# Kernel optimization log

Measured on AMD Instinct MI355X. Metric: run time of the kernel, lower is better.

## Reference

```python
import jax, jax.numpy as jnp
import numpy as np

N = 100000      # nodes
E = 1600000     # edges
F = 64          # num_features
C = 10          # num_classes
L = 4           # num_layers
B = 128         # graphs in batch


def setup_inputs() -> dict:
    key = jax.random.key(0)
    ks = jax.random.split(key, 8)
    x = jax.random.normal(ks[0], (N, F), dtype=jnp.float32)
    edge_index = jax.random.randint(ks[1], (2, E), 0, N, dtype=jnp.int64)
    batch = jnp.sort(jax.random.randint(ks[2], (N,), 0, B, dtype=jnp.int64))
    scale = 1.0 / jnp.sqrt(jnp.float32(F))
    W1s = jax.random.normal(ks[3], (L, F, F), dtype=jnp.float32) * scale
    W2s = jax.random.normal(ks[4], (L, F, F), dtype=jnp.float32) * scale
    fc_w = jax.random.normal(ks[5], (C, F), dtype=jnp.float32) * scale
    fc_b = jax.random.normal(ks[6], (C,), dtype=jnp.float32) * 0.01
    return {"x": x, "edge_index": edge_index, "batch": batch,
            "W1s": W1s, "W2s": W2s, "fc_w": fc_w, "fc_b": fc_b}


def reference(x, edge_index, batch, W1s, W2s, fc_w, fc_b):
    src, dst = edge_index[0], edge_index[1]
    h = x
    for l in range(L):  # small fixed layer count
        # GINConv, eps=0: (1+eps)*x + sum of neighbor features (gather + scatter-add)
        agg = jax.ops.segment_sum(h[src], dst, num_segments=N)
        h = agg + h
        # MLP([F,F,F], bias=False, plain_last=False, act=sigmoid): two linears, each followed by sigmoid
        h = jax.nn.sigmoid(h @ W1s[l])
        h = jax.nn.sigmoid(h @ W2s[l])
    # global_add_pool over graphs in the batch
    xr = jax.ops.segment_sum(h, batch, num_segments=B)  # [B, F]
    logits = xr @ fc_w.T + fc_b                          # [B, C]
    return jax.nn.log_softmax(logits, axis=1), xr
```

## Files before the change

kernel.cpp:

```cpp
#include <hip/hip_runtime.h>
#include <hip/hip_bf16.h>

#define NN 100000
#define NE 1600000
#define FF 64
#define NC 10
#define NL 4
#define NB 128
#define LDST 72
#define CAP 48
#define NW 196
#define WCAPE 8704
#define NCHUNK ((NE + 1023) / 1024)
#define XF_BLOCKS (NN * FF / 2048)
#define CONV_BLOCKS (2 * NL * FF * FF / 256)

typedef __attribute__((ext_vector_type(8))) short short8;
typedef __attribute__((ext_vector_type(8))) unsigned short ushort8;
typedef __attribute__((ext_vector_type(4))) float f32x4;
typedef __attribute__((ext_vector_type(2))) float f32x2;

static __device__ __forceinline__ unsigned short f2bf(float x) {
  unsigned int u = __float_as_uint(x);
  unsigned int r = (u + 0x7fffu + ((u >> 16) & 1u)) >> 16;
  return (unsigned short)r;
}
static __device__ __forceinline__ float bf2f(unsigned short u) {
  return __uint_as_float(((unsigned int)u) << 16);
}
static __device__ __forceinline__ uint2 pack_f8(const float* a) {
  int w0 = __builtin_amdgcn_cvt_pk_fp8_f32(a[0], a[1], 0, false);
  w0 = __builtin_amdgcn_cvt_pk_fp8_f32(a[2], a[3], w0, true);
  int w1 = __builtin_amdgcn_cvt_pk_fp8_f32(a[4], a[5], 0, false);
  w1 = __builtin_amdgcn_cvt_pk_fp8_f32(a[6], a[7], w1, true);
  return make_uint2((unsigned)w0, (unsigned)w1);
}
static __device__ __forceinline__ void acc8(f32x2* a, uint2 v) {
#if __has_builtin(__builtin_amdgcn_cvt_pk_f32_fp8)
  a[0] += __builtin_amdgcn_cvt_pk_f32_fp8((int)v.x, false);
  a[1] += __builtin_amdgcn_cvt_pk_f32_fp8((int)v.x, true);
  a[2] += __builtin_amdgcn_cvt_pk_f32_fp8((int)v.y, false);
  a[3] += __builtin_amdgcn_cvt_pk_f32_fp8((int)v.y, true);
#else
  a[0][0] += __builtin_amdgcn_cvt_f32_fp8((int)v.x, 0);
  a[0][1] += __builtin_amdgcn_cvt_f32_fp8((int)v.x, 1);
  a[1][0] += __builtin_amdgcn_cvt_f32_fp8((int)v.x, 2);
  a[1][1] += __builtin_amdgcn_cvt_f32_fp8((int)v.x, 3);
  a[2][0] += __builtin_amdgcn_cvt_f32_fp8((int)v.y, 0);
  a[2][1] += __builtin_amdgcn_cvt_f32_fp8((int)v.y, 1);
  a[3][0] += __builtin_amdgcn_cvt_f32_fp8((int)v.y, 2);
  a[3][1] += __builtin_amdgcn_cvt_f32_fp8((int)v.y, 3);
#endif
}
static __device__ __forceinline__ unsigned char f2f8(float v) {
  return (unsigned char)(__builtin_amdgcn_cvt_pk_fp8_f32(v, v, 0, false) & 0xff);
}

__global__ __launch_bounds__(256) void prep_kernel(
    const float* __restrict__ x, const float* __restrict__ W1s,
    const float* __restrict__ W2s, uint2* __restrict__ xf8,
    unsigned short* __restrict__ Wt, int* __restrict__ wcnt,
    uint2* __restrict__ hf8a, uint2* __restrict__ hf8b,
    float* __restrict__ xr) {
  int b = blockIdx.x;
  if (b < XF_BLOCKS) {
    int t = b * 256 + threadIdx.x;
    size_t base = (size_t)t * 8;
    float4 a = *(const float4*)(x + base);
    float4 c = *(const float4*)(x + base + 4);
    float f[8] = {a.x, a.y, a.z, a.w, c.x, c.y, c.z, c.w};
    xf8[t] = pack_f8(f);
  } else if (b < XF_BLOCKS + CONV_BLOCKS) {
    int t = (b - XF_BLOCKS) * 256 + threadIdx.x;
    int mat = t >> 12, idx = t & 4095;
    int k = idx >> 6, n = idx & 63;
    int l = mat >> 1;
    const float* W = (mat & 1) ? (W2s + (size_t)l * FF * FF) : (W1s + (size_t)l * FF * FF);
    Wt[(size_t)mat * FF * FF + n * FF + k] = f2bf(W[k * FF + n]);
  } else {
    int c = threadIdx.x;
    float4 z = make_float4(0.f, 0.f, 0.f, 0.f);
    #pragma unroll
    for (int k = 0; k < 8; ++k)
      *(float4*)(xr + c * 32 + k * 4) = z;
    if (c < NW) wcnt[c] = 0;
    if (c < 8) {
      xf8[(size_t)NN * 8 + c] = make_uint2(0, 0);
      hf8a[(size_t)NN * 8 + c] = make_uint2(0, 0);
      hf8b[(size_t)NN * 8 + c] = make_uint2(0, 0);
    }
  }
}

__global__ __launch_bounds__(256) void binB_kernel(const int* __restrict__ src,
                                                   const int* __restrict__ dst,
                                                   int* __restrict__ wcnt,
                                                   unsigned int* __restrict__ ebuf) {
  __shared__ int lcnt[NW];
  __shared__ int lbase[NW];
  int t = threadIdx.x;
  int base = blockIdx.x * 1024 + t * 4;
  int d[4], s[4], wj[4];
  bool v[4];
  #pragma unroll
  for (int j = 0; j < 4; ++j) {
    int e = base + j;
    v[j] = (e < NE);
    d[j] = v[j] ? dst[e] : 0;
    s[j] = v[j] ? src[e] : 0;
    wj[j] = d[j] >> 9;
  }
  for (int i = t; i < NW; i += 256) lcnt[i] = 0;
  __syncthreads();
  #pragma unroll
  for (int j = 0; j < 4; ++j)
    if (v[j]) atomicAdd(&lcnt[wj[j]], 1);
  __syncthreads();
  if (t < NW) {
    lbase[t] = atomicAdd(&wcnt[t], lcnt[t]);
    lcnt[t] = 0;
  }
  __syncthreads();
  #pragma unroll
  for (int j = 0; j < 4; ++j) {
    if (v[j]) {
      int pos = lbase[wj[j]] + atomicAdd(&lcnt[wj[j]], 1);
      if (pos < WCAPE)
        ebuf[(size_t)wj[j] * WCAPE + pos] =
            ((unsigned)(d[j] & 511) << 17) | (unsigned)s[j];
    }
  }
}

__global__ __launch_bounds__(256) void fillC_kernel(const unsigned int* __restrict__ ebuf,
                                                    const int* __restrict__ wcnt,
                                                    int* __restrict__ csr,
                                                    int* __restrict__ deg) {
  __shared__ int cur[512];
  int b = blockIdx.x;
  int t = threadIdx.x;
  int n0 = b << 9;
  cur[t] = 0; cur[t + 256] = 0;
  __syncthreads();
  int cnt = min(wcnt[b], WCAPE);
  const unsigned int* ep = ebuf + (size_t)b * WCAPE;
  for (int i = t; i < cnt; i += 256) {
    unsigned int e = ep[i];
    int dl = e >> 17;
    int s = (int)(e & 0x1ffffu);
    int slot = atomicAdd(&cur[dl], 1);
    if (slot < CAP) csr[(n0 + dl) * CAP + slot] = s;
  }
  __syncthreads();
  #pragma unroll
  for (int p = 0; p < 2; ++p) {
    int nl = p * 256 + t;
    int node = n0 + nl;
    if (node < NN) {
      int c = min(cur[nl], CAP);
      deg[node] = c;
      int end = (c + 3) & ~3;
      for (; c < end; ++c) csr[node * CAP + c] = NN;
    }
  }
}

__global__ __launch_bounds__(256) void layer_kernel(
    const uint2* __restrict__ hin8, const int* __restrict__ csr,
    const int* __restrict__ deg, const unsigned short* __restrict__ Wt,
    uint2* __restrict__ hout8, const int* __restrict__ batch,
    float* __restrict__ xr, int last) {
  __shared__ __align__(16) unsigned short uL[64 * LDST];
  __shared__ __align__(8) unsigned char fb[64 * 64];
  int t = threadIdx.x;
  int row0 = blockIdx.x * 64;
  int lane = t & 63, w = t >> 6;
  int j = lane & 7;
  int gnode = lane >> 3;

  #pragma unroll
  for (int pass = 0; pass < 2; ++pass) {
    int r = w * 16 + pass * 8 + gnode;
    int node = row0 + r;
    f32x2 a[4] = {{0.f, 0.f}, {0.f, 0.f}, {0.f, 0.f}, {0.f, 0.f}};
    if (node < NN) {
      const uint2* hp = hin8 + j;
      acc8(a, hp[(size_t)node * 8]);
      int i = node * CAP;
      int dg = deg[node];
      int endp = i + ((dg + 3) & ~3);
      for (; i + 8 <= endp; i += 8) {
        int4 x0 = *(const int4*)(csr + i);
        int4 x1 = *(const int4*)(csr + i + 4);
        uint2 r0 = hp[(size_t)x0.x * 8];
        uint2 r1 = hp[(size_t)x0.y * 8];
        uint2 r2 = hp[(size_t)x0.z * 8];
        uint2 r3 = hp[(size_t)x0.w * 8];
        uint2 r4 = hp[(size_t)x1.x * 8];
        uint2 r5 = hp[(size_t)x1.y * 8];
        uint2 r6 = hp[(size_t)x1.z * 8];
        uint2 r7 = hp[(size_t)x1.w * 8];
        acc8(a, r0); acc8(a, r1); acc8(a, r2); acc8(a, r3);
        acc8(a, r4); acc8(a, r5); acc8(a, r6); acc8(a, r7);
      }
      if (i < endp) {
        int4 x0 = *(const int4*)(csr + i);
        uint2 r0 = hp[(size_t)x0.x * 8];
        uint2 r1 = hp[(size_t)x0.y * 8];
        uint2 r2 = hp[(size_t)x0.z * 8];
        uint2 r3 = hp[(size_t)x0.w * 8];
        acc8(a, r0); acc8(a, r1); acc8(a, r2); acc8(a, r3);
      }
    }
    ushort8 u;
    #pragma unroll
    for (int kk = 0; kk < 8; ++kk) u[kk] = f2bf(a[kk >> 1][kk & 1]);
    *(ushort8*)(&uL[r * LDST + j * 8]) = u;
  }

  __builtin_amdgcn_sched_barrier(0);

  int m = lane & 15, q = lane >> 4;
  short8 b1[4][2], b2[4][2];
  #pragma unroll
  for (int c4 = 0; c4 < 4; ++c4) {
    #pragma unroll
    for (int s = 0; s < 2; ++s) {
      b1[c4][s] = *(const short8*)(Wt + (c4 * 16 + m) * FF + s * 32 + q * 8);
      b2[c4][s] = *(const short8*)(Wt + FF * FF + (c4 * 16 + m) * FF + s * 32 + q * 8);
    }
  }

  f32x4 acc[4] = {{0,0,0,0},{0,0,0,0},{0,0,0,0},{0,0,0,0}};
  #pragma unroll
  for (int s = 0; s < 2; ++s) {
    short8 a = *(const short8*)(&uL[(w * 16 + m) * LDST + s * 32 + q * 8]);
    #pragma unroll
    for (int c4 = 0; c4 < 4; ++c4)
      acc[c4] = __builtin_amdgcn_mfma_f32_16x16x32_bf16(a, b1[c4][s], acc[c4], 0, 0, 0);
  }
  #pragma unroll
  for (int c4 = 0; c4 < 4; ++c4) {
    #pragma unroll
    for (int i = 0; i < 4; ++i) {
      int r = w * 16 + q * 4 + i;
      float sgv = 1.f / (1.f + __expf(-acc[c4][i]));
      uL[r * LDST + c4 * 16 + m] = f2bf(sgv);
    }
  }

  f32x4 acc2[4] = {{0,0,0,0},{0,0,0,0},{0,0,0,0},{0,0,0,0}};
  #pragma unroll
  for (int s = 0; s < 2; ++s) {
    short8 a = *(const short8*)(&uL[(w * 16 + m) * LDST + s * 32 + q * 8]);
    #pragma unroll
    for (int c4 = 0; c4 < 4; ++c4)
      acc2[c4] = __builtin_amdgcn_mfma_f32_16x16x32_bf16(a, b2[c4][s], acc2[c4], 0, 0, 0);
  }
  if (last) {
    #pragma unroll
    for (int c4 = 0; c4 < 4; ++c4) {
      #pragma unroll
      for (int i = 0; i < 4; ++i) {
        int r = w * 16 + q * 4 + i;
        float sgv = 1.f / (1.f + __expf(-acc2[c4][i]));
        uL[r * LDST + c4 * 16 + m] = f2bf(sgv);
      }
    }
    int r0 = w * 16;
    int node0 = row0 + r0;
    if (node0 < NN) {
      float pacc = 0.f;
      int cur = batch[node0];
      #pragma unroll
      for (int r = 0; r < 16; ++r) {
        int node = node0 + r;
        if (node < NN) {
          int bb = batch[node];
          if (bb != cur) {
            unsafeAtomicAdd(&xr[(size_t)cur * FF + lane], pacc);
            pacc = 0.f; cur = bb;
          }
          pacc += bf2f(uL[(r0 + r) * LDST + lane]);
        }
      }
      unsafeAtomicAdd(&xr[(size_t)cur * FF + lane], pacc);
    }
  } else {
    #pragma unroll
    for (int c4 = 0; c4 < 4; ++c4) {
      #pragma unroll
      for (int i = 0; i < 4; ++i) {
        int r = w * 16 + q * 4 + i;
        float sgv = 1.f / (1.f + __expf(-acc2[c4][i]));
        fb[r * 64 + c4 * 16 + m] = f2f8(sgv);
      }
    }
    #pragma unroll
    for (int pass = 0; pass < 2; ++pass) {
      int r = w * 16 + pass * 8 + gnode;
      int node = row0 + r;
      if (node < NN) {
        uint2 v = *(const uint2*)(fb + r * 64 + j * 8);
        hout8[(size_t)node * 8 + j] = v;
      }
    }
  }
}

__global__ __launch_bounds__(64) void head_kernel(
    const float* __restrict__ xr, const float* __restrict__ fcw,
    const float* __restrict__ fcb, float* __restrict__ out) {
  int b = blockIdx.x, lane = threadIdx.x;
  float v = xr[(size_t)b * FF + lane];
  out[NB * NC + (size_t)b * FF + lane] = v;
  float logit[NC];
  #pragma unroll
  for (int c = 0; c < NC; ++c) {
    float s = v * fcw[c * FF + lane];
    #pragma unroll
    for (int o = 32; o > 0; o >>= 1) s += __shfl_xor(s, o, 64);
    logit[c] = s + fcb[c];
  }
  float mx = logit[0];
  #pragma unroll
  for (int c = 1; c < NC; ++c) mx = fmaxf(mx, logit[c]);
  float se = 0.f;
  #pragma unroll
  for (int c = 0; c < NC; ++c) se += expf(logit[c] - mx);
  float lse = logf(se);
  if (lane < NC) out[b * NC + lane] = logit[lane] - mx - lse;
}

extern "C" void kernel_launch(void* const* d_in, const int* in_sizes, int n_in,
                              void* d_out, int out_size, void* d_ws, size_t ws_size,
                              hipStream_t stream) {
  const float* x     = (const float*)d_in[0];
  const int*   ei    = (const int*)d_in[1];
  const int*   batch = (const int*)d_in[2];
  const float* W1s   = (const float*)d_in[3];
  const float* W2s   = (const float*)d_in[4];
  const float* fcw   = (const float*)d_in[5];
  const float* fcb   = (const float*)d_in[6];
  float* out = (float*)d_out;

  char* p = (char*)d_ws;
  uint2* xf8  = (uint2*)p; p += (size_t)(NN + 1) * 8 * 8;
  uint2* hf8a = (uint2*)p; p += (size_t)(NN + 1) * 8 * 8;
  uint2* hf8b = (uint2*)p; p += (size_t)(NN + 1) * 8 * 8;
  int* csr    = (int*)p;   p += (size_t)NN * CAP * 4;
  unsigned int* ebuf = (unsigned int*)p; p += (size_t)NW * WCAPE * 4;
  int* deg    = (int*)p;   p += (size_t)NN * 4;
  int* wcnt   = (int*)p;   p += (size_t)((NW + 63) & ~63) * 4;
  float* xr   = (float*)p; p += (size_t)NB * FF * 4;
  unsigned short* Wtall = (unsigned short*)p; p += (size_t)2 * NL * FF * FF * 2;

  const int* src = ei;
  const int* dst = ei + NE;

  prep_kernel<<<XF_BLOCKS + CONV_BLOCKS + 1, 256, 0, stream>>>(
      x, W1s, W2s, xf8, Wtall, wcnt, hf8a, hf8b, xr);

  binB_kernel<<<NCHUNK, 256, 0, stream>>>(src, dst, wcnt, ebuf);
  fillC_kernel<<<NW, 256, 0, stream>>>(ebuf, wcnt, csr, deg);

  int layer_blocks = (NN + 63) / 64;
  const uint2* chain_in[NL]  = {xf8, hf8a, hf8b, hf8a};
  uint2*       chain_out[NL] = {hf8a, hf8b, hf8a, hf8b};
  for (int l = 0; l < NL; ++l) {
    int last = (l == NL - 1) ? 1 : 0;
    layer_kernel<<<layer_blocks, 256, 0, stream>>>(chain_in[l], csr, deg,
        Wtall + (size_t)l * 2 * FF * FF, chain_out[l], batch, xr, last);
  }

  head_kernel<<<NB, 64, 0, stream>>>(xr, fcw, fcb, out);
}
```

Measured before the change: 290.7 us.

## Widen gathers to 16-byte rows and enlarge binning/fill blocks

The layer kernel now gives each node 4 lanes that each load 16 bytes of the fp8 row, instead of 8 lanes loading 8 bytes, so all 64 rows are covered in one pass rather than two. The edge loop shrinks to 4-edge steps. binB now handles 8192 edges per 1024-thread block with vectorized int4 loads of src and dst, cutting global atomics on wcnt, and fillC runs 1024 threads per bin. The aim is fewer, wider memory transactions and less atomic traffic. The cost is fewer gathers in flight per wavefront, a shorter unroll, and larger blocks that may lower occupancy.

New measurement: 269.2 us. 1.08x faster.

```diff
diff --git a/kernel.cpp b/kernel.cpp
--- a/kernel.cpp
+++ b/kernel.cpp
@@ -11,7 +11,7 @@
 #define CAP 48
 #define NW 196
 #define WCAPE 8704
-#define NCHUNK ((NE + 1023) / 1024)
+#define BINB_BLOCKS ((NE + 8191) / 8192)
 #define XF_BLOCKS (NN * FF / 2048)
 #define CONV_BLOCKS (2 * NL * FF * FF / 256)
 
@@ -35,22 +35,27 @@
   w1 = __builtin_amdgcn_cvt_pk_fp8_f32(a[6], a[7], w1, true);
   return make_uint2((unsigned)w0, (unsigned)w1);
 }
-static __device__ __forceinline__ void acc8(f32x2* a, uint2 v) {
+static __device__ __forceinline__ void acc8w(f32x2* a, unsigned int x,
+                                             unsigned int y) {
 #if __has_builtin(__builtin_amdgcn_cvt_pk_f32_fp8)
-  a[0] += __builtin_amdgcn_cvt_pk_f32_fp8((int)v.x, false);
-  a[1] += __builtin_amdgcn_cvt_pk_f32_fp8((int)v.x, true);
-  a[2] += __builtin_amdgcn_cvt_pk_f32_fp8((int)v.y, false);
-  a[3] += __builtin_amdgcn_cvt_pk_f32_fp8((int)v.y, true);
+  a[0] += __builtin_amdgcn_cvt_pk_f32_fp8((int)x, false);
+  a[1] += __builtin_amdgcn_cvt_pk_f32_fp8((int)x, true);
+  a[2] += __builtin_amdgcn_cvt_pk_f32_fp8((int)y, false);
+  a[3] += __builtin_amdgcn_cvt_pk_f32_fp8((int)y, true);
 #else
-  a[0][0] += __builtin_amdgcn_cvt_f32_fp8((int)v.x, 0);
-  a[0][1] += __builtin_amdgcn_cvt_f32_fp8((int)v.x, 1);
-  a[1][0] += __builtin_amdgcn_cvt_f32_fp8((int)v.x, 2);
-  a[1][1] += __builtin_amdgcn_cvt_f32_fp8((int)v.x, 3);
-  a[2][0] += __builtin_amdgcn_cvt_f32_fp8((int)v.y, 0);
-  a[2][1] += __builtin_amdgcn_cvt_f32_fp8((int)v.y, 1);
-  a[3][0] += __builtin_amdgcn_cvt_f32_fp8((int)v.y, 2);
-  a[3][1] += __builtin_amdgcn_cvt_f32_fp8((int)v.y, 3);
+  a[0][0] += __builtin_amdgcn_cvt_f32_fp8((int)x, 0);
+  a[0][1] += __builtin_amdgcn_cvt_f32_fp8((int)x, 1);
+  a[1][0] += __builtin_amdgcn_cvt_f32_fp8((int)x, 2);
+  a[1][1] += __builtin_amdgcn_cvt_f32_fp8((int)x, 3);
+  a[2][0] += __builtin_amdgcn_cvt_f32_fp8((int)y, 0);
+  a[2][1] += __builtin_amdgcn_cvt_f32_fp8((int)y, 1);
+  a[3][0] += __builtin_amdgcn_cvt_f32_fp8((int)y, 2);
+  a[3][1] += __builtin_amdgcn_cvt_f32_fp8((int)y, 3);
 #endif
+}
+static __device__ __forceinline__ void acc16(f32x2* a, uint4 v) {
+  acc8w(a, v.x, v.y);
+  acc8w(a + 4, v.z, v.w);
 }
 static __device__ __forceinline__ unsigned char f2f8(float v) {
   return (unsigned char)(__builtin_amdgcn_cvt_pk_fp8_f32(v, v, 0, false) & 0xff);
@@ -92,28 +97,38 @@
   }
 }
 
-__global__ __launch_bounds__(256) void binB_kernel(const int* __restrict__ src,
-                                                   const int* __restrict__ dst,
-                                                   int* __restrict__ wcnt,
-                                                   unsigned int* __restrict__ ebuf) {
+__global__ __launch_bounds__(1024) void binB_kernel(const int* __restrict__ src,
+                                                    const int* __restrict__ dst,
+                                                    int* __restrict__ wcnt,
+                                                    unsigned int* __restrict__ ebuf) {
   __shared__ int lcnt[NW];
   __shared__ int lbase[NW];
   int t = threadIdx.x;
-  int base = blockIdx.x * 1024 + t * 4;
-  int d[4], s[4], wj[4];
-  bool v[4];
-  #pragma unroll
-  for (int j = 0; j < 4; ++j) {
-    int e = base + j;
-    v[j] = (e < NE);
-    d[j] = v[j] ? dst[e] : 0;
-    s[j] = v[j] ? src[e] : 0;
-    wj[j] = d[j] >> 9;
-  }
-  for (int i = t; i < NW; i += 256) lcnt[i] = 0;
-  __syncthreads();
-  #pragma unroll
-  for (int j = 0; j < 4; ++j)
+  int base = blockIdx.x * 8192 + t * 8;
+  int d[8], s[8], wj[8];
+  bool v[8];
+  if (base + 8 <= NE) {
+    *(int4*)(&d[0]) = *(const int4*)(dst + base);
+    *(int4*)(&d[4]) = *(const int4*)(dst + base + 4);
+    *(int4*)(&s[0]) = *(const int4*)(src + base);
+    *(int4*)(&s[4]) = *(const int4*)(src + base + 4);
+    #pragma unroll
+    for (int j = 0; j < 8; ++j) v[j] = true;
+  } else {
+    #pragma unroll
+    for (int j = 0; j < 8; ++j) {
+      int e = base + j;
+      v[j] = (e < NE);
+      d[j] = v[j] ? dst[e] : 0;
+      s[j] = v[j] ? src[e] : 0;
+    }
+  }
+  #pragma unroll
+  for (int j = 0; j < 8; ++j) wj[j] = d[j] >> 9;
+  if (t < NW) lcnt[t] = 0;
+  __syncthreads();
+  #pragma unroll
+  for (int j = 0; j < 8; ++j)
     if (v[j]) atomicAdd(&lcnt[wj[j]], 1);
   __syncthreads();
   if (t < NW) {
@@ -122,7 +137,7 @@
   }
   __syncthreads();
   #pragma unroll
-  for (int j = 0; j < 4; ++j) {
+  for (int j = 0; j < 8; ++j) {
     if (v[j]) {
       int pos = lbase[wj[j]] + atomicAdd(&lcnt[wj[j]], 1);
       if (pos < WCAPE)
@@ -132,19 +147,19 @@
   }
 }
 
-__global__ __launch_bounds__(256) void fillC_kernel(const unsigned int* __restrict__ ebuf,
-                                                    const int* __restrict__ wcnt,
-                                                    int* __restrict__ csr,
-                                                    int* __restrict__ deg) {
+__global__ __launch_bounds__(1024) void fillC_kernel(const unsigned int* __restrict__ ebuf,
+                                                     const int* __restrict__ wcnt,
+                                                     int* __restrict__ csr,
+                                                     int* __restrict__ deg) {
   __shared__ int cur[512];
   int b = blockIdx.x;
   int t = threadIdx.x;
   int n0 = b << 9;
-  cur[t] = 0; cur[t + 256] = 0;
+  if (t < 512) cur[t] = 0;
   __syncthreads();
   int cnt = min(wcnt[b], WCAPE);
   const unsigned int* ep = ebuf + (size_t)b * WCAPE;
-  for (int i = t; i < cnt; i += 256) {
+  for (int i = t; i < cnt; i += 1024) {
     unsigned int e = ep[i];
     int dl = e >> 17;
     int s = (int)(e & 0x1ffffu);
@@ -152,12 +167,10 @@
     if (slot < CAP) csr[(n0 + dl) * CAP + slot] = s;
   }
   __syncthreads();
-  #pragma unroll
-  for (int p = 0; p < 2; ++p) {
-    int nl = p * 256 + t;
-    int node = n0 + nl;
+  if (t < 512) {
+    int node = n0 + t;
     if (node < NN) {
-      int c = min(cur[nl], CAP);
+      int c = min(cur[t], CAP);
       deg[node] = c;
       int end = (c + 3) & ~3;
       for (; c < end; ++c) csr[node * CAP + c] = NN;
@@ -171,51 +184,40 @@
     uint2* __restrict__ hout8, const int* __restrict__ batch,
     float* __restrict__ xr, int last) {
   __shared__ __align__(16) unsigned short uL[64 * LDST];
-  __shared__ __align__(8) unsigned char fb[64 * 64];
+  __shared__ __align__(16) unsigned char fb[64 * 64];
   int t = threadIdx.x;
   int row0 = blockIdx.x * 64;
   int lane = t & 63, w = t >> 6;
-  int j = lane & 7;
-  int gnode = lane >> 3;
-
-  #pragma unroll
-  for (int pass = 0; pass < 2; ++pass) {
-    int r = w * 16 + pass * 8 + gnode;
+  int j2 = lane & 3;
+  int gnode = lane >> 2;
+
+  {
+    int r = w * 16 + gnode;
     int node = row0 + r;
-    f32x2 a[4] = {{0.f, 0.f}, {0.f, 0.f}, {0.f, 0.f}, {0.f, 0.f}};
+    f32x2 a[8] = {{0.f,0.f},{0.f,0.f},{0.f,0.f},{0.f,0.f},
+                  {0.f,0.f},{0.f,0.f},{0.f,0.f},{0.f,0.f}};
+    const uint4* hp4 = (const uint4*)hin8 + j2;
     if (node < NN) {
-      const uint2* hp = hin8 + j;
-      acc8(a, hp[(size_t)node * 8]);
+      acc16(a, hp4[(size_t)node * 4]);
       int i = node * CAP;
       int dg = deg[node];
       int endp = i + ((dg + 3) & ~3);
-      for (; i + 8 <= endp; i += 8) {
+      for (; i < endp; i += 4) {
         int4 x0 = *(const int4*)(csr + i);
-        int4 x1 = *(const int4*)(csr + i + 4);
-        uint2 r0 = hp[(size_t)x0.x * 8];
-        uint2 r1 = hp[(size_t)x0.y * 8];
-        uint2 r2 = hp[(size_t)x0.z * 8];
-        uint2 r3 = hp[(size_t)x0.w * 8];
-        uint2 r4 = hp[(size_t)x1.x * 8];
-        uint2 r5 = hp[(size_t)x1.y * 8];
-        uint2 r6 = hp[(size_t)x1.z * 8];
-        uint2 r7 = hp[(size_t)x1.w * 8];
-        acc8(a, r0); acc8(a, r1); acc8(a, r2); acc8(a, r3);
-        acc8(a, r4); acc8(a, r5); acc8(a, r6); acc8(a, r7);
-      }
-      if (i < endp) {
-        int4 x0 = *(const int4*)(csr + i);
-        uint2 r0 = hp[(size_t)x0.x * 8];
-        uint2 r1 = hp[(size_t)x0.y * 8];
-        uint2 r2 = hp[(size_t)x0.z * 8];
-        uint2 r3 = hp[(size_t)x0.w * 8];
-        acc8(a, r0); acc8(a, r1); acc8(a, r2); acc8(a, r3);
-      }
-    }
-    ushort8 u;
-    #pragma unroll
-    for (int kk = 0; kk < 8; ++kk) u[kk] = f2bf(a[kk >> 1][kk & 1]);
-    *(ushort8*)(&uL[r * LDST + j * 8]) = u;
+        uint4 r0 = hp4[(size_t)x0.x * 4];
+        uint4 r1 = hp4[(size_t)x0.y * 4];
+        uint4 r2 = hp4[(size_t)x0.z * 4];
+        uint4 r3 = hp4[(size_t)x0.w * 4];
+        acc16(a, r0); acc16(a, r1); acc16(a, r2); acc16(a, r3);
+      }
+    }
+    ushort8 u0, u1;
+    #pragma unroll
+    for (int kk = 0; kk < 8; ++kk) u0[kk] = f2bf(a[kk >> 1][kk & 1]);
+    #pragma unroll
+    for (int kk = 0; kk < 8; ++kk) u1[kk] = f2bf(a[4 + (kk >> 1)][kk & 1]);
+    *(ushort8*)(&uL[r * LDST + j2 * 16]) = u0;
+    *(ushort8*)(&uL[r * LDST + j2 * 16 + 8]) = u1;
   }
 
   __builtin_amdgcn_sched_barrier(0);
@@ -296,13 +298,13 @@
         fb[r * 64 + c4 * 16 + m] = f2f8(sgv);
       }
     }
-    #pragma unroll
-    for (int pass = 0; pass < 2; ++pass) {
-      int r = w * 16 + pass * 8 + gnode;
+    {
+      int r = w * 16 + gnode;
       int node = row0 + r;
       if (node < NN) {
-        uint2 v = *(const uint2*)(fb + r * 64 + j * 8);
-        hout8[(size_t)node * 8 + j] = v;
+        uint4 v = *(const uint4*)(fb + r * 64 + j2 * 16);
+        uint4* hout4 = (uint4*)hout8;
+        hout4[(size_t)node * 4 + j2] = v;
       }
     }
   }
@@ -361,8 +363,8 @@
   prep_kernel<<<XF_BLOCKS + CONV_BLOCKS + 1, 256, 0, stream>>>(
       x, W1s, W2s, xf8, Wtall, wcnt, hf8a, hf8b, xr);
 
-  binB_kernel<<<NCHUNK, 256, 0, stream>>>(src, dst, wcnt, ebuf);
-  fillC_kernel<<<NW, 256, 0, stream>>>(ebuf, wcnt, csr, deg);
+  binB_kernel<<<BINB_BLOCKS, 1024, 0, stream>>>(src, dst, wcnt, ebuf);
+  fillC_kernel<<<NW, 1024, 0, stream>>>(ebuf, wcnt, csr, deg);
 
   int layer_blocks = (NN + 63) / 64;
   const uint2* chain_in[NL]  = {xf8, hf8a, hf8b, hf8a};
```

## Halve nodes per layer block, widen binning blocks to 1024 threads with vector loads

Applied to the files above, without the earlier changes.

Each layer block now aggregates 32 nodes instead of 64. The 16 MFMA rows per wave are half padding, so the block count doubles and the gather phase gets more parallelism, at the cost of wasted matrix work. The binning kernel now uses 1024-thread blocks that handle 8 edges per thread with int4 loads, which cuts global atomics on the bucket counters. The CSR fill kernel also uses 1024 threads. The per-node bounds checks are dropped, which relies on NN being divisible by 32.

Measured after the change: 299.6 us. 3.1% more time.

```diff
diff --git a/kernel.cpp b/kernel.cpp
--- a/kernel.cpp
+++ b/kernel.cpp
@@ -11,9 +11,10 @@
 #define CAP 48
 #define NW 196
 #define WCAPE 8704
-#define NCHUNK ((NE + 1023) / 1024)
+#define BINB_BLOCKS ((NE + 8191) / 8192)
 #define XF_BLOCKS (NN * FF / 2048)
 #define CONV_BLOCKS (2 * NL * FF * FF / 256)
+#define LAYER_BLOCKS (NN / 32)
 
 typedef __attribute__((ext_vector_type(8))) short short8;
 typedef __attribute__((ext_vector_type(8))) unsigned short ushort8;
@@ -92,28 +93,38 @@
   }
 }
 
-__global__ __launch_bounds__(256) void binB_kernel(const int* __restrict__ src,
-                                                   const int* __restrict__ dst,
-                                                   int* __restrict__ wcnt,
-                                                   unsigned int* __restrict__ ebuf) {
+__global__ __launch_bounds__(1024) void binB_kernel(const int* __restrict__ src,
+                                                    const int* __restrict__ dst,
+                                                    int* __restrict__ wcnt,
+                                                    unsigned int* __restrict__ ebuf) {
   __shared__ int lcnt[NW];
   __shared__ int lbase[NW];
   int t = threadIdx.x;
-  int base = blockIdx.x * 1024 + t * 4;
-  int d[4], s[4], wj[4];
-  bool v[4];
-  #pragma unroll
-  for (int j = 0; j < 4; ++j) {
-    int e = base + j;
-    v[j] = (e < NE);
-    d[j] = v[j] ? dst[e] : 0;
-    s[j] = v[j] ? src[e] : 0;
-    wj[j] = d[j] >> 9;
-  }
-  for (int i = t; i < NW; i += 256) lcnt[i] = 0;
-  __syncthreads();
-  #pragma unroll
-  for (int j = 0; j < 4; ++j)
+  int base = blockIdx.x * 8192 + t * 8;
+  int d[8], s[8], wj[8];
+  bool v[8];
+  if (base + 8 <= NE) {
+    *(int4*)(&d[0]) = *(const int4*)(dst + base);
+    *(int4*)(&d[4]) = *(const int4*)(dst + base + 4);
+    *(int4*)(&s[0]) = *(const int4*)(src + base);
+    *(int4*)(&s[4]) = *(const int4*)(src + base + 4);
+    #pragma unroll
+    for (int j = 0; j < 8; ++j) v[j] = true;
+  } else {
+    #pragma unroll
+    for (int j = 0; j < 8; ++j) {
+      int e = base + j;
+      v[j] = (e < NE);
+      d[j] = v[j] ? dst[e] : 0;
+      s[j] = v[j] ? src[e] : 0;
+    }
+  }
+  #pragma unroll
+  for (int j = 0; j < 8; ++j) wj[j] = d[j] >> 9;
+  if (t < NW) lcnt[t] = 0;
+  __syncthreads();
+  #pragma unroll
+  for (int j = 0; j < 8; ++j)
     if (v[j]) atomicAdd(&lcnt[wj[j]], 1);
   __syncthreads();
   if (t < NW) {
@@ -122,7 +133,7 @@
   }
   __syncthreads();
   #pragma unroll
-  for (int j = 0; j < 4; ++j) {
+  for (int j = 0; j < 8; ++j) {
     if (v[j]) {
       int pos = lbase[wj[j]] + atomicAdd(&lcnt[wj[j]], 1);
       if (pos < WCAPE)
@@ -132,19 +143,19 @@
   }
 }
 
-__global__ __launch_bounds__(256) void fillC_kernel(const unsigned int* __restrict__ ebuf,
-                                                    const int* __restrict__ wcnt,
-                                                    int* __restrict__ csr,
-                                                    int* __restrict__ deg) {
+__global__ __launch_bounds__(1024) void fillC_kernel(const unsigned int* __restrict__ ebuf,
+                                                     const int* __restrict__ wcnt,
+                                                     int* __restrict__ csr,
+                                                     int* __restrict__ deg) {
   __shared__ int cur[512];
   int b = blockIdx.x;
   int t = threadIdx.x;
   int n0 = b << 9;
-  cur[t] = 0; cur[t + 256] = 0;
+  if (t < 512) cur[t] = 0;
   __syncthreads();
   int cnt = min(wcnt[b], WCAPE);
   const unsigned int* ep = ebuf + (size_t)b * WCAPE;
-  for (int i = t; i < cnt; i += 256) {
+  for (int i = t; i < cnt; i += 1024) {
     unsigned int e = ep[i];
     int dl = e >> 17;
     int s = (int)(e & 0x1ffffu);
@@ -152,12 +163,10 @@
     if (slot < CAP) csr[(n0 + dl) * CAP + slot] = s;
   }
   __syncthreads();
-  #pragma unroll
-  for (int p = 0; p < 2; ++p) {
-    int nl = p * 256 + t;
-    int node = n0 + nl;
+  if (t < 512) {
+    int node = n0 + t;
     if (node < NN) {
-      int c = min(cur[nl], CAP);
+      int c = min(cur[t], CAP);
       deg[node] = c;
       int end = (c + 3) & ~3;
       for (; c < end; ++c) csr[node * CAP + c] = NN;
@@ -171,51 +180,48 @@
     uint2* __restrict__ hout8, const int* __restrict__ batch,
     float* __restrict__ xr, int last) {
   __shared__ __align__(16) unsigned short uL[64 * LDST];
-  __shared__ __align__(8) unsigned char fb[64 * 64];
+  __shared__ __align__(16) unsigned char fb[64 * 64];
   int t = threadIdx.x;
-  int row0 = blockIdx.x * 64;
+  int row0 = blockIdx.x * 32;
   int lane = t & 63, w = t >> 6;
-  int j = lane & 7;
+  int j3 = lane & 7;
   int gnode = lane >> 3;
 
-  #pragma unroll
-  for (int pass = 0; pass < 2; ++pass) {
-    int r = w * 16 + pass * 8 + gnode;
-    int node = row0 + r;
+  {
+    int r = w * 16 + gnode;
+    int node = row0 + w * 8 + gnode;
     f32x2 a[4] = {{0.f, 0.f}, {0.f, 0.f}, {0.f, 0.f}, {0.f, 0.f}};
-    if (node < NN) {
-      const uint2* hp = hin8 + j;
-      acc8(a, hp[(size_t)node * 8]);
-      int i = node * CAP;
-      int dg = deg[node];
-      int endp = i + ((dg + 3) & ~3);
-      for (; i + 8 <= endp; i += 8) {
-        int4 x0 = *(const int4*)(csr + i);
-        int4 x1 = *(const int4*)(csr + i + 4);
-        uint2 r0 = hp[(size_t)x0.x * 8];
-        uint2 r1 = hp[(size_t)x0.y * 8];
-        uint2 r2 = hp[(size_t)x0.z * 8];
-        uint2 r3 = hp[(size_t)x0.w * 8];
-        uint2 r4 = hp[(size_t)x1.x * 8];
-        uint2 r5 = hp[(size_t)x1.y * 8];
-        uint2 r6 = hp[(size_t)x1.z * 8];
-        uint2 r7 = hp[(size_t)x1.w * 8];
-        acc8(a, r0); acc8(a, r1); acc8(a, r2); acc8(a, r3);
-        acc8(a, r4); acc8(a, r5); acc8(a, r6); acc8(a, r7);
-      }
-      if (i < endp) {
-        int4 x0 = *(const int4*)(csr + i);
-        uint2 r0 = hp[(size_t)x0.x * 8];
-        uint2 r1 = hp[(size_t)x0.y * 8];
-        uint2 r2 = hp[(size_t)x0.z * 8];
-        uint2 r3 = hp[(size_t)x0.w * 8];
-        acc8(a, r0); acc8(a, r1); acc8(a, r2); acc8(a, r3);
-      }
+    const uint2* hp = hin8 + j3;
+    acc8(a, hp[(size_t)node * 8]);
+    int i = node * CAP;
+    int dg = deg[node];
+    int endp = i + ((dg + 3) & ~3);
+    for (; i + 8 <= endp; i += 8) {
+      int4 x0 = *(const int4*)(csr + i);
+      int4 x1 = *(const int4*)(csr + i + 4);
+      uint2 r0 = hp[(size_t)x0.x * 8];
+      uint2 r1 = hp[(size_t)x0.y * 8];
+      uint2 r2 = hp[(size_t)x0.z * 8];
+      uint2 r3 = hp[(size_t)x0.w * 8];
+      uint2 r4 = hp[(size_t)x1.x * 8];
+      uint2 r5 = hp[(size_t)x1.y * 8];
+      uint2 r6 = hp[(size_t)x1.z * 8];
+      uint2 r7 = hp[(size_t)x1.w * 8];
+      acc8(a, r0); acc8(a, r1); acc8(a, r2); acc8(a, r3);
+      acc8(a, r4); acc8(a, r5); acc8(a, r6); acc8(a, r7);
+    }
+    if (i < endp) {
+      int4 x0 = *(const int4*)(csr + i);
+      uint2 r0 = hp[(size_t)x0.x * 8];
+      uint2 r1 = hp[(size_t)x0.y * 8];
+      uint2 r2 = hp[(size_t)x0.z * 8];
+      uint2 r3 = hp[(size_t)x0.w * 8];
+      acc8(a, r0); acc8(a, r1); acc8(a, r2); acc8(a, r3);
     }
     ushort8 u;
     #pragma unroll
     for (int kk = 0; kk < 8; ++kk) u[kk] = f2bf(a[kk >> 1][kk & 1]);
-    *(ushort8*)(&uL[r * LDST + j * 8]) = u;
+    *(ushort8*)(&uL[r * LDST + j3 * 8]) = u;
   }
 
   __builtin_amdgcn_sched_barrier(0);
@@ -267,22 +273,19 @@
         uL[r * LDST + c4 * 16 + m] = f2bf(sgv);
       }
     }
-    int r0 = w * 16;
-    int node0 = row0 + r0;
-    if (node0 < NN) {
+    int node0 = row0 + w * 8;
+    {
       float pacc = 0.f;
       int cur = batch[node0];
       #pragma unroll
-      for (int r = 0; r < 16; ++r) {
+      for (int r = 0; r < 8; ++r) {
         int node = node0 + r;
-        if (node < NN) {
-          int bb = batch[node];
-          if (bb != cur) {
-            unsafeAtomicAdd(&xr[(size_t)cur * FF + lane], pacc);
-            pacc = 0.f; cur = bb;
-          }
-          pacc += bf2f(uL[(r0 + r) * LDST + lane]);
+        int bb = batch[node];
+        if (bb != cur) {
+          unsafeAtomicAdd(&xr[(size_t)cur * FF + lane], pacc);
+          pacc = 0.f; cur = bb;
         }
+        pacc += bf2f(uL[(w * 16 + r) * LDST + lane]);
       }
       unsafeAtomicAdd(&xr[(size_t)cur * FF + lane], pacc);
     }
@@ -296,14 +299,11 @@
         fb[r * 64 + c4 * 16 + m] = f2f8(sgv);
       }
     }
-    #pragma unroll
-    for (int pass = 0; pass < 2; ++pass) {
-      int r = w * 16 + pass * 8 + gnode;
-      int node = row0 + r;
-      if (node < NN) {
-        uint2 v = *(const uint2*)(fb + r * 64 + j * 8);
-        hout8[(size_t)node * 8 + j] = v;
-      }
+    {
+      int r = w * 16 + gnode;
+      int node = row0 + w * 8 + gnode;
+      uint2 v = *(const uint2*)(fb + r * 64 + j3 * 8);
+      hout8[(size_t)node * 8 + j3] = v;
     }
   }
 }
@@ -361,15 +361,14 @@
   prep_kernel<<<XF_BLOCKS + CONV_BLOCKS + 1, 256, 0, stream>>>(
       x, W1s, W2s, xf8, Wtall, wcnt, hf8a, hf8b, xr);
 
-  binB_kernel<<<NCHUNK, 256, 0, stream>>>(src, dst, wcnt, ebuf);
-  fillC_kernel<<<NW, 256, 0, stream>>>(ebuf, wcnt, csr, deg);
-
-  int layer_blocks = (NN + 63) / 64;
+  binB_kernel<<<BINB_BLOCKS, 1024, 0, stream>>>(src, dst, wcnt, ebuf);
+  fillC_kernel<<<NW, 1024, 0, stream>>>(ebuf, wcnt, csr, deg);
+
   const uint2* chain_in[NL]  = {xf8, hf8a, hf8b, hf8a};
   uint2*       chain_out[NL] = {hf8a, hf8b, hf8a, hf8b};
   for (int l = 0; l < NL; ++l) {
     int last = (l == NL - 1) ? 1 : 0;
-    layer_kernel<<<layer_blocks, 256, 0, stream>>>(chain_in[l], csr, deg,
+    layer_kernel<<<LAYER_BLOCKS, 256, 0, stream>>>(chain_in[l], csr, deg,
         Wtall + (size_t)l * 2 * FF * FF, chain_out[l], batch, xr, last);
   }
 
```
